# Optimization experiments

Hardware: AMD Instinct MI355X
Metric: run time of the kernel (lower is better)

## Reference

```python
import jax, jax.numpy as jnp
import numpy as np

IN_FEATURES = 1024
OUT_FEATURES = 256
NUM_KNOTS = 10
SPLINE_ORDER = 3
NUM_BASIS = NUM_KNOTS + SPLINE_ORDER  # 13
EPS = 1e-8


def setup_inputs() -> dict:
    key = jax.random.key(0)
    k1, k2 = jax.random.split(key)
    x = jax.random.normal(k1, (8192, IN_FEATURES), dtype=jnp.float32)
    spline_coeffs = jax.random.normal(
        k2, (OUT_FEATURES, IN_FEATURES, NUM_BASIS), dtype=jnp.float32) * 0.1
    knots = jnp.linspace(-1.0, 1.0, NUM_KNOTS + 2 * SPLINE_ORDER, dtype=jnp.float32)
    return {"x": x, "spline_coeffs": spline_coeffs, "knots": knots}


def _basis_functions(x, knots):
    # x: (B, I) already tanh-normalized; returns (B, I, NUM_BASIS)
    xc = jnp.clip(x, -1.0, 1.0)[..., None]          # (B, I, 1)
    left = knots[:NUM_BASIS - 1]                     # (nb-1,)
    center = knots[1:NUM_BASIS]                      # (nb-1,)
    right = knots[2:NUM_BASIS + 1]                   # (nb-1,)  (i+2 < len(knots) always)
    mask_l = (xc >= left) & (xc < center)
    mask_r = (xc >= center) & (xc < right)
    up = mask_l.astype(xc.dtype) * (xc - left) / (center - left + EPS)
    down = mask_r.astype(xc.dtype) * (right - xc) / (right - center + EPS)
    b = up + down                                    # (B, I, nb-1)
    # last basis column is never written in the original loop -> zeros
    return jnp.pad(b, ((0, 0), (0, 0), (0, 1)))


def reference(x, spline_coeffs, knots):
    x_norm = jnp.tanh(x)
    basis = _basis_functions(x_norm, knots)          # (B, I, K)
    # output[b, j] = sum_i sum_k basis[b, i, k] * coeffs[j, i, k]
    return jnp.einsum('bik,jik->bj', basis, spline_coeffs)
```

## Files before the change

kernel.cpp:

```cpp
#include <hip/hip_runtime.h>
#include <cstdint>
#include <cstddef>


typedef _Float16 half2_v __attribute__((ext_vector_type(2)));
typedef __fp16  fp16x2  __attribute__((ext_vector_type(2)));
typedef _Float16 f16x8 __attribute__((ext_vector_type(8)));
typedef float f32x4 __attribute__((ext_vector_type(4)));

__device__ __forceinline__ half2_v u32_as_h2(uint32_t u) {
  union { uint32_t u; half2_v h; } c; c.u = u; return c.h;
}
__device__ __forceinline__ uint32_t h2_as_u32(half2_v h) {
  union { uint32_t u; half2_v h; } c; c.h = h; return c.u;
}
__device__ __forceinline__ half2_v cvt_pk_h2(float a, float b) {
  union { fp16x2 f; half2_v h; } c;
  c.f = __builtin_amdgcn_cvt_pkrtz(a, b);
  return c.h;
}
__device__ __forceinline__ float dot2f(half2_v a, half2_v b, float c) {
#if __has_builtin(__builtin_amdgcn_fdot2)
  return __builtin_amdgcn_fdot2(a, b, c, false);
#else
  return c + (float)a[0] * (float)b[0] + (float)a[1] * (float)b[1];
#endif
}
__device__ __forceinline__ uint16_t f16_bits(float v) {
  union { _Float16 h; uint16_t u; } c; c.h = (_Float16)v; return c.u;
}

__device__ __forceinline__ float fast_tanhf(float v) {
  const float e = __expf(2.0f * v);
  return 1.0f - 2.0f / (e + 1.0f);
}

#define KSTEP 0.13333333333333333f
#define KINV  7.49999943750004f
__device__ __forceinline__ void kan_weights(float xin, float& w0, float& w1, int& lo) {
  float xc = fast_tanhf(xin);
  xc = fminf(fmaxf(xc, -1.0f), 1.0f);
  int m = (int)((xc + 1.0f) * 7.5f);
  m = min(max(m, 0), 14);
  const float k0 = fmaf((float)m, KSTEP, -1.0f);
  const float up = (xc - k0) * KINV;
  const float dn = (k0 + KSTEP - xc) * KINV;
  w0 = (m == 0) ? up : ((m <= 12) ? dn : 0.0f);
  w1 = (m >= 1 && m <= 11) ? up : 0.0f;
  lo = min(max(m - 1, 0), 11);
}

__device__ __forceinline__ void load_lds16(const void* g, void* l) {
  __builtin_amdgcn_global_load_lds((const __attribute__((address_space(1))) void*)g,
                                   (__attribute__((address_space(3))) void*)l, 16, 0, 0);
}

#define GMM 8192
#define GNN 256
#define KI  12
#define GK2 (1024 * KI)
#define KSPL2 2
#define IPER (1024 / KSPL2)
#define BM2 64
#define BN2 256
#define NSG 64
#define NSTEP 192
#define AS_STRIDE 208
#define AS_SG (64 * AS_STRIDE)
#define OUT_ELEMS (8192 * 256)

__global__ __launch_bounds__(256)
void kan_prep_B2(const float* __restrict__ coef, uint32_t* __restrict__ B2,
                 float4* __restrict__ outz, int zero_out) {
  const int tid = blockIdx.x * 256 + threadIdx.x;
  const float* cp = coef + (size_t)tid * 13;
  uint32_t w[6];
#pragma unroll
  for (int q = 0; q < 6; ++q) w[q] = h2_as_u32(cvt_pk_h2(cp[2 * q], cp[2 * q + 1]));
  uint2* p = (uint2*)(B2 + (size_t)tid * 6);
  p[0] = make_uint2(w[0], w[1]);
  p[1] = make_uint2(w[2], w[3]);
  p[2] = make_uint2(w[4], w[5]);
  if (zero_out) {
    const float4 z = make_float4(0.f, 0.f, 0.f, 0.f);
    outz[tid] = z;
    outz[tid + 262144] = z;
  }
}

__global__ __launch_bounds__(256)
void kan_reduce2(const float4* __restrict__ part, float4* __restrict__ out) {
  const int i = blockIdx.x * 256 + threadIdx.x;
  out[i] = make_float4(part[i].x + part[i + OUT_ELEMS / 4].x,
                       part[i].y + part[i + OUT_ELEMS / 4].y,
                       part[i].z + part[i + OUT_ELEMS / 4].z,
                       part[i].w + part[i + OUT_ELEMS / 4].w);
}

__global__ __launch_bounds__(512, 2)
void kan_gemm13(const float* __restrict__ x, const _Float16* __restrict__ B2,
                float* __restrict__ out, float* __restrict__ part, int mode) {
  __shared__ __align__(16) char Bs[4][16384];
  __shared__ __align__(16) char As[2][AS_SG];
  char* BsP = (char*)Bs;
  char* AsP = (char*)As;

  const int t    = threadIdx.x;
  const int lane = t & 63;
  const int wv   = t >> 6;
  const int wm   = (wv & 1) * 32;
  const int wn   = (wv >> 1) * 64;
  const int fr   = lane & 15;
  const int fq   = lane >> 4;
  const int m0   = blockIdx.z * BM2;
  const int i00  = blockIdx.x * IPER;

  const int a_base = (wm + fr) * AS_STRIDE + fq * 16;
  const int b_base = (wn + fr) * 64 + ((fq ^ (fr & 3)) * 16);

  f32x4 acc[2][4];
#pragma unroll
  for (int a = 0; a < 2; ++a)
#pragma unroll
    for (int b = 0; b < 4; ++b) acc[a][b] = (f32x4){0.f, 0.f, 0.f, 0.f};

  const int srow0 = t >> 2, sc0 = t & 3;
  const int srow1 = 128 + (t >> 2);
  const _Float16* sp0 = B2 + (size_t)srow0 * GK2 + (size_t)i00 * KI
                        + ((sc0 ^ (srow0 & 3)) * 8);
  const _Float16* sp1 = B2 + (size_t)srow1 * GK2 + (size_t)i00 * KI
                        + ((sc0 ^ (srow1 & 3)) * 8);

  const int xrow  = t & 63;
  const int i_loc = t >> 6;
  const float* xptr = x + (size_t)(m0 + xrow) * 1024 + i00 + i_loc;
  const int exp_off = xrow * AS_STRIDE + i_loc * 24;

  auto expand1 = [&](int dst, float xv) {
    float w0, w1; int lo;
    kan_weights(xv, w0, w1, lo);
    const uint32_t wp  = (uint32_t)f16_bits(w0) | ((uint32_t)f16_bits(w1) << 16);
    const uint32_t wlo = (lo & 1) ? (wp << 16) : wp;
    const uint32_t whi = (lo & 1) ? (wp >> 16) : 0u;
    const int w   = lo >> 1;
    const int wn1 = (w + 1 > 5) ? 5 : (w + 1);
    char* rb = AsP + dst + exp_off;
    if ((i_loc & 1) == 0) {
      *(uint4*)(rb)      = make_uint4(0u, 0u, 0u, 0u);
      *(uint2*)(rb + 16) = make_uint2(0u, 0u);
    } else {
      *(uint2*)(rb)      = make_uint2(0u, 0u);
      *(uint4*)(rb + 8)  = make_uint4(0u, 0u, 0u, 0u);
    }
    *(uint32_t*)(rb + wn1 * 4) = whi;
    *(uint32_t*)(rb + w * 4)   = wlo;
  };

  float cx, nx = 0.f;

  {
    const float ex = xptr[0];
    load_lds16(sp0, BsP + t * 16);
    load_lds16(sp1, BsP + 8192 + t * 16);
    sp0 += 32; sp1 += 32;
    load_lds16(sp0, BsP + 16384 + t * 16);
    load_lds16(sp1, BsP + 16384 + 8192 + t * 16);
    sp0 += 32; sp1 += 32;
    expand1(0, ex);
    cx = xptr[8];
  }
  asm volatile("s_waitcnt vmcnt(2) lgkmcnt(0)" ::: "memory");
  __builtin_amdgcn_s_barrier();
  __builtin_amdgcn_sched_barrier(0);

#define GRANP(U, PH, XPF)                                                     \
  {                                                                           \
    const int g = 12 * B + 3 * (U) + (PH);                                    \
    const char* Asrc = AsP + ((U) & 1) * AS_SG;                               \
    f16x8 af0 = *(const f16x8*)(Asrc + a_base + (PH) * 64);                   \
    f16x8 af1 = *(const f16x8*)(Asrc + a_base + (PH) * 64 + 16 * AS_STRIDE);  \
    load_lds16(sp0, BsP + ((3 * (U) + (PH) + 2) & 3) * 16384 + t * 16);       \
    load_lds16(sp1, BsP + ((3 * (U) + (PH) + 2) & 3) * 16384 + 8192 + t * 16);\
    { const int adv = (g + 3 <= NSTEP - 1) ? 32 : 0; sp0 += adv; sp1 += adv; }\
    XPF                                                                       \
    if ((PH) == 0 && (4 * B + (U)) < NSG - 1)                                 \
      expand1((((U) + 1) & 1) * AS_SG, cx);                                   \
    asm volatile("s_waitcnt vmcnt(3) lgkmcnt(0)" ::: "memory");               \
    __builtin_amdgcn_s_barrier();                                             \
    __builtin_amdgcn_sched_barrier(0);                                        \
    __builtin_amdgcn_s_setprio(1);                                            \
    _Pragma("unroll")                                                         \
    for (int ni = 0; ni < 4; ++ni) {                                          \
      const f16x8 bf = *(const f16x8*)(BsP + ((3 * (U) + (PH)) & 3) * 16384   \
                                       + b_base + ni * 1024);                 \
      acc[0][ni] = __builtin_amdgcn_mfma_f32_16x16x32_f16(af0, bf, acc[0][ni], 0, 0, 0); \
      acc[1][ni] = __builtin_amdgcn_mfma_f32_16x16x32_f16(af1, bf, acc[1][ni], 0, 0, 0); \
    }                                                                         \
    __builtin_amdgcn_s_setprio(0);                                            \
  }

#define SGBODY(U)                                                             \
  {                                                                           \
    const int sgp = 4 * B + (U) + 2;                                          \
    const int sgn = (sgp < NSG) ? sgp : (NSG - 1);                            \
    GRANP(U, 0, { })                                                          \
    GRANP(U, 1, { nx = xptr[8 * sgn]; })                                      \
    GRANP(U, 2, { })                                                          \
    cx = nx;                                                                  \
  }

  for (int B = 0; B < 16; ++B) {
    SGBODY(0)
    SGBODY(1)
    SGBODY(2)
    SGBODY(3)
  }
#undef SGBODY
#undef GRANP

  if (mode) {
    float* pb = part + (size_t)blockIdx.x * OUT_ELEMS;
#pragma unroll
    for (int q = 0; q < 2; ++q) {
      const int gr = m0 + wm + q * 16 + fq * 4;
#pragma unroll
      for (int ni = 0; ni < 4; ++ni) {
        const int gc = wn + ni * 16 + fr;
#pragma unroll
        for (int r = 0; r < 4; ++r)
          pb[(size_t)(gr + r) * GNN + gc] = acc[q][ni][r];
      }
    }
  } else {
#pragma unroll
    for (int q = 0; q < 2; ++q) {
      const int gr = m0 + wm + q * 16 + fq * 4;
#pragma unroll
      for (int ni = 0; ni < 4; ++ni) {
        const int gc = wn + ni * 16 + fr;
#pragma unroll
        for (int r = 0; r < 4; ++r)
          atomicAdd(&out[(size_t)(gr + r) * GNN + gc], acc[q][ni][r]);
      }
    }
  }
}

#define TI 8
#define BT 256
#define JT 32
#define ISPL 2
#define IRANGE (1024 / ISPL)

__global__ __launch_bounds__(256)
void kan_dot2(const float* __restrict__ x, const float* __restrict__ coef,
              float* __restrict__ out) {
  __shared__ uint32_t Plds[TI * 12 * JT];
  const int t    = threadIdx.x;
  const int b    = blockIdx.x * BT + t;
  const int j0   = blockIdx.y * JT;
  const int cbeg = blockIdx.z * (IRANGE / TI);

  float acc[JT];
#pragma unroll
  for (int q = 0; q < JT; ++q) acc[q] = 0.0f;

  const int s_jj   = t & 31;
  const int s_iloc = t >> 5;

  for (int c = cbeg; c < cbeg + IRANGE / TI; ++c) {
    const int i0 = c * TI;
    __syncthreads();
    {
      const float* cp0 = coef + ((size_t)(j0 + s_jj) * 1024 + (i0 + s_iloc)) * 13;
      float cv[13];
#pragma unroll
      for (int s = 0; s < 13; ++s) cv[s] = cp0[s];
#pragma unroll
      for (int r = 0; r < 12; ++r) {
        half2_v h; h[0] = (_Float16)cv[r]; h[1] = (_Float16)cv[r + 1];
        const int slot = ((s_jj >> 2) + r) & 7;
        Plds[(s_iloc * 12 + r) * 32 + slot * 4 + (s_jj & 3)] = h2_as_u32(h);
      }
    }
    uint32_t wr[TI]; int lor[TI];
    {
      const float* xr = x + (size_t)b * 1024 + i0;
      const float4 xa = *(const float4*)(xr);
      const float4 xb = *(const float4*)(xr + 4);
      const float xv[TI] = {xa.x, xa.y, xa.z, xa.w, xb.x, xb.y, xb.z, xb.w};
#pragma unroll
      for (int q = 0; q < TI; ++q) {
        float w0, w1; int lo;
        kan_weights(xv[q], w0, w1, lo);
        wr[q] = (uint32_t)f16_bits(w0) | ((uint32_t)f16_bits(w1) << 16);
        lor[q] = lo;
      }
    }
    __syncthreads();

    const uint4* P4 = (const uint4*)Plds;
#pragma unroll
    for (int ii = 0; ii < TI; ++ii) {
      const half2_v hw = u32_as_h2(wr[ii]);
      const int lo = lor[ii];
      const int base = (ii * 12 + lo) * 8;
#pragma unroll
      for (int g = 0; g < 8; ++g) {
        const uint4 v = P4[base + ((g + lo) & 7)];
        acc[4 * g + 0] = dot2f(hw, u32_as_h2(v.x), acc[4 * g + 0]);
        acc[4 * g + 1] = dot2f(hw, u32_as_h2(v.y), acc[4 * g + 1]);
        acc[4 * g + 2] = dot2f(hw, u32_as_h2(v.z), acc[4 * g + 2]);
        acc[4 * g + 3] = dot2f(hw, u32_as_h2(v.w), acc[4 * g + 3]);
      }
    }
  }

  float* orow = out + (size_t)b * 256 + j0;
#pragma unroll
  for (int q = 0; q < JT; ++q) atomicAdd(orow + q, acc[q]);
}

extern "C" void kernel_launch(void* const* d_in, const int* in_sizes, int n_in,
                              void* d_out, int out_size, void* d_ws, size_t ws_size,
                              hipStream_t stream) {
  const float* x     = (const float*)d_in[0];
  const float* coef  = (const float*)d_in[1];
  float* out = (float*)d_out;

  const size_t b2_bytes   = (size_t)GNN * GK2 * 2;
  const size_t part_off   = b2_bytes;
  const size_t part_bytes = (size_t)KSPL2 * OUT_ELEMS * 4;

  if (ws_size >= part_off + part_bytes) {
    _Float16* B2 = (_Float16*)d_ws;
    float* part  = (float*)((char*)d_ws + part_off);
    kan_prep_B2<<<1024, 256, 0, stream>>>(coef, (uint32_t*)B2, (float4*)out, 0);
    dim3 grid(KSPL2, 1, GMM / BM2);
    kan_gemm13<<<grid, 512, 0, stream>>>(x, B2, out, part, 1);
    kan_reduce2<<<OUT_ELEMS / 4 / 256, 256, 0, stream>>>((const float4*)part,
                                                         (float4*)out);
  } else if (ws_size >= b2_bytes) {
    _Float16* B2 = (_Float16*)d_ws;
    kan_prep_B2<<<1024, 256, 0, stream>>>(coef, (uint32_t*)B2, (float4*)out, 1);
    dim3 grid(KSPL2, 1, GMM / BM2);
    kan_gemm13<<<grid, 512, 0, stream>>>(x, B2, out, nullptr, 0);
  } else {
    (void)hipMemsetAsync(out, 0, (size_t)out_size * sizeof(float), stream);
    dim3 grid(8192 / BT, 256 / JT, ISPL);
    kan_dot2<<<grid, 256, 0, stream>>>(x, coef, out);
  }
}
```

Measured before the change: 187.5 us.

## Split N across blocks: 256-thread 64x128 tiles with four waves each

Each GEMM block now covers a 64x128 output tile with 256 threads instead of 64x256 with 512 threads, and the grid gains an N-split dimension. Each wave computes all 64 rows by 32 columns, so it issues four A fragment loads and reuses each B fragment across four MFMAs. The basis expansion of x is spread over two phases because there are fewer threads. The aims are more blocks per CU, smaller LDS per block, better occupancy and latency hiding, and the x prefetch now runs after the barrier. The cost is that every x row is expanded twice (once per N half) and A is reread more often from LDS.

```diff
diff --git a/kernel.cpp b/kernel.cpp
--- a/kernel.cpp
+++ b/kernel.cpp
@@ -60,12 +60,14 @@
 #define KI  12
 #define GK2 (1024 * KI)
 #define KSPL2 2
+#define NSPL2 2
 #define IPER (1024 / KSPL2)
 #define BM2 64
-#define BN2 256
+#define BN2 128
 #define NSG 64
 #define NSTEP 192
-#define AS_STRIDE 208
+#define BS_TILE 8192
+#define AS_STRIDE 200
 #define AS_SG (64 * AS_STRIDE)
 #define OUT_ELEMS (8192 * 256)
 
@@ -97,10 +99,10 @@
                        part[i].w + part[i + OUT_ELEMS / 4].w);
 }
 
-__global__ __launch_bounds__(512, 2)
-void kan_gemm13(const float* __restrict__ x, const _Float16* __restrict__ B2,
+__global__ __launch_bounds__(256, 4)
+void kan_gemm14(const float* __restrict__ x, const _Float16* __restrict__ B2,
                 float* __restrict__ out, float* __restrict__ part, int mode) {
-  __shared__ __align__(16) char Bs[4][16384];
+  __shared__ __align__(16) char Bs[4][BS_TILE];
   __shared__ __align__(16) char As[2][AS_SG];
   char* BsP = (char*)Bs;
   char* AsP = (char*)As;
@@ -108,35 +110,34 @@
   const int t    = threadIdx.x;
   const int lane = t & 63;
   const int wv   = t >> 6;
-  const int wm   = (wv & 1) * 32;
-  const int wn   = (wv >> 1) * 64;
+  const int wn   = wv * 32;
   const int fr   = lane & 15;
   const int fq   = lane >> 4;
   const int m0   = blockIdx.z * BM2;
+  const int n0   = blockIdx.y * BN2;
   const int i00  = blockIdx.x * IPER;
 
-  const int a_base = (wm + fr) * AS_STRIDE + fq * 16;
+  const int a_base = fr * AS_STRIDE + fq * 16;
   const int b_base = (wn + fr) * 64 + ((fq ^ (fr & 3)) * 16);
 
-  f32x4 acc[2][4];
-#pragma unroll
-  for (int a = 0; a < 2; ++a)
-#pragma unroll
-    for (int b = 0; b < 4; ++b) acc[a][b] = (f32x4){0.f, 0.f, 0.f, 0.f};
+  f32x4 acc[4][2];
+#pragma unroll
+  for (int a = 0; a < 4; ++a)
+#pragma unroll
+    for (int b = 0; b < 2; ++b) acc[a][b] = (f32x4){0.f, 0.f, 0.f, 0.f};
 
   const int srow0 = t >> 2, sc0 = t & 3;
-  const int srow1 = 128 + (t >> 2);
-  const _Float16* sp0 = B2 + (size_t)srow0 * GK2 + (size_t)i00 * KI
+  const int srow1 = 64 + (t >> 2);
+  const _Float16* sp0 = B2 + (size_t)(n0 + srow0) * GK2 + (size_t)i00 * KI
                         + ((sc0 ^ (srow0 & 3)) * 8);
-  const _Float16* sp1 = B2 + (size_t)srow1 * GK2 + (size_t)i00 * KI
+  const _Float16* sp1 = B2 + (size_t)(n0 + srow1) * GK2 + (size_t)i00 * KI
                         + ((sc0 ^ (srow1 & 3)) * 8);
 
   const int xrow  = t & 63;
   const int i_loc = t >> 6;
   const float* xptr = x + (size_t)(m0 + xrow) * 1024 + i00 + i_loc;
-  const int exp_off = xrow * AS_STRIDE + i_loc * 24;
-
-  auto expand1 = [&](int dst, float xv) {
+
+  auto expand1 = [&](int dst, float xv, int il) {
     float w0, w1; int lo;
     kan_weights(xv, w0, w1, lo);
     const uint32_t wp  = (uint32_t)f16_bits(w0) | ((uint32_t)f16_bits(w1) << 16);
@@ -144,8 +145,8 @@
     const uint32_t whi = (lo & 1) ? (wp >> 16) : 0u;
     const int w   = lo >> 1;
     const int wn1 = (w + 1 > 5) ? 5 : (w + 1);
-    char* rb = AsP + dst + exp_off;
-    if ((i_loc & 1) == 0) {
+    char* rb = AsP + dst + xrow * AS_STRIDE + il * 24;
+    if ((il & 1) == 0) {
       *(uint4*)(rb)      = make_uint4(0u, 0u, 0u, 0u);
       *(uint2*)(rb + 16) = make_uint2(0u, 0u);
     } else {
@@ -156,20 +157,23 @@
     *(uint32_t*)(rb + w * 4)   = wlo;
   };
 
-  float cx, nx = 0.f;
+  float cxa, cxb, nxa = 0.f, nxb = 0.f;
 
   {
-    const float ex = xptr[0];
+    const float exa = xptr[0];
+    const float exb = xptr[4];
     load_lds16(sp0, BsP + t * 16);
-    load_lds16(sp1, BsP + 8192 + t * 16);
+    load_lds16(sp1, BsP + (256 + t) * 16);
     sp0 += 32; sp1 += 32;
-    load_lds16(sp0, BsP + 16384 + t * 16);
-    load_lds16(sp1, BsP + 16384 + 8192 + t * 16);
+    load_lds16(sp0, BsP + BS_TILE + t * 16);
+    load_lds16(sp1, BsP + BS_TILE + (256 + t) * 16);
     sp0 += 32; sp1 += 32;
-    expand1(0, ex);
-    cx = xptr[8];
-  }
-  asm volatile("s_waitcnt vmcnt(2) lgkmcnt(0)" ::: "memory");
+    expand1(0, exa, i_loc);
+    expand1(0, exb, i_loc + 4);
+    cxa = xptr[8];
+    cxb = xptr[12];
+  }
+  asm volatile("s_waitcnt vmcnt(0) lgkmcnt(0)" ::: "memory");
   __builtin_amdgcn_s_barrier();
   __builtin_amdgcn_sched_barrier(0);
 
@@ -179,22 +183,28 @@
     const char* Asrc = AsP + ((U) & 1) * AS_SG;                               \
     f16x8 af0 = *(const f16x8*)(Asrc + a_base + (PH) * 64);                   \
     f16x8 af1 = *(const f16x8*)(Asrc + a_base + (PH) * 64 + 16 * AS_STRIDE);  \
-    load_lds16(sp0, BsP + ((3 * (U) + (PH) + 2) & 3) * 16384 + t * 16);       \
-    load_lds16(sp1, BsP + ((3 * (U) + (PH) + 2) & 3) * 16384 + 8192 + t * 16);\
+    f16x8 af2 = *(const f16x8*)(Asrc + a_base + (PH) * 64 + 32 * AS_STRIDE);  \
+    f16x8 af3 = *(const f16x8*)(Asrc + a_base + (PH) * 64 + 48 * AS_STRIDE);  \
+    load_lds16(sp0, BsP + ((3 * (U) + (PH) + 2) & 3) * BS_TILE + t * 16);     \
+    load_lds16(sp1, BsP + ((3 * (U) + (PH) + 2) & 3) * BS_TILE + (256 + t) * 16); \
     { const int adv = (g + 3 <= NSTEP - 1) ? 32 : 0; sp0 += adv; sp1 += adv; }\
-    XPF                                                                       \
     if ((PH) == 0 && (4 * B + (U)) < NSG - 1)                                 \
-      expand1((((U) + 1) & 1) * AS_SG, cx);                                   \
-    asm volatile("s_waitcnt vmcnt(3) lgkmcnt(0)" ::: "memory");               \
+      expand1((((U) + 1) & 1) * AS_SG, cxa, i_loc);                           \
+    if ((PH) == 1 && (4 * B + (U)) < NSG - 1)                                 \
+      expand1((((U) + 1) & 1) * AS_SG, cxb, i_loc + 4);                       \
+    asm volatile("s_waitcnt vmcnt(4) lgkmcnt(0)" ::: "memory");               \
     __builtin_amdgcn_s_barrier();                                             \
     __builtin_amdgcn_sched_barrier(0);                                        \
+    XPF                                                                       \
     __builtin_amdgcn_s_setprio(1);                                            \
     _Pragma("unroll")                                                         \
-    for (int ni = 0; ni < 4; ++ni) {                                          \
-      const f16x8 bf = *(const f16x8*)(BsP + ((3 * (U) + (PH)) & 3) * 16384   \
+    for (int ni = 0; ni < 2; ++ni) {                                          \
+      const f16x8 bf = *(const f16x8*)(BsP + ((3 * (U) + (PH)) & 3) * BS_TILE \
                                        + b_base + ni * 1024);                 \
       acc[0][ni] = __builtin_amdgcn_mfma_f32_16x16x32_f16(af0, bf, acc[0][ni], 0, 0, 0); \
       acc[1][ni] = __builtin_amdgcn_mfma_f32_16x16x32_f16(af1, bf, acc[1][ni], 0, 0, 0); \
+      acc[2][ni] = __builtin_amdgcn_mfma_f32_16x16x32_f16(af2, bf, acc[2][ni], 0, 0, 0); \
+      acc[3][ni] = __builtin_amdgcn_mfma_f32_16x16x32_f16(af3, bf, acc[3][ni], 0, 0, 0); \
     }                                                                         \
     __builtin_amdgcn_s_setprio(0);                                            \
   }
@@ -204,9 +214,9 @@
     const int sgp = 4 * B + (U) + 2;                                          \
     const int sgn = (sgp < NSG) ? sgp : (NSG - 1);                            \
     GRANP(U, 0, { })                                                          \
-    GRANP(U, 1, { nx = xptr[8 * sgn]; })                                      \
+    GRANP(U, 1, { nxa = xptr[8 * sgn]; nxb = xptr[8 * sgn + 4]; })            \
     GRANP(U, 2, { })                                                          \
-    cx = nx;                                                                  \
+    cxa = nxa; cxb = nxb;                                                     \
   }
 
   for (int B = 0; B < 16; ++B) {
@@ -221,11 +231,11 @@
   if (mode) {
     float* pb = part + (size_t)blockIdx.x * OUT_ELEMS;
 #pragma unroll
-    for (int q = 0; q < 2; ++q) {
-      const int gr = m0 + wm + q * 16 + fq * 4;
-#pragma unroll
-      for (int ni = 0; ni < 4; ++ni) {
-        const int gc = wn + ni * 16 + fr;
+    for (int q = 0; q < 4; ++q) {
+      const int gr = m0 + q * 16 + fq * 4;
+#pragma unroll
+      for (int ni = 0; ni < 2; ++ni) {
+        const int gc = n0 + wn + ni * 16 + fr;
 #pragma unroll
         for (int r = 0; r < 4; ++r)
           pb[(size_t)(gr + r) * GNN + gc] = acc[q][ni][r];
@@ -233,11 +243,11 @@
     }
   } else {
 #pragma unroll
-    for (int q = 0; q < 2; ++q) {
-      const int gr = m0 + wm + q * 16 + fq * 4;
-#pragma unroll
-      for (int ni = 0; ni < 4; ++ni) {
-        const int gc = wn + ni * 16 + fr;
+    for (int q = 0; q < 4; ++q) {
+      const int gr = m0 + q * 16 + fq * 4;
+#pragma unroll
+      for (int ni = 0; ni < 2; ++ni) {
+        const int gc = n0 + wn + ni * 16 + fr;
 #pragma unroll
         for (int r = 0; r < 4; ++r)
           atomicAdd(&out[(size_t)(gr + r) * GNN + gc], acc[q][ni][r]);
@@ -336,15 +346,15 @@
     _Float16* B2 = (_Float16*)d_ws;
     float* part  = (float*)((char*)d_ws + part_off);
     kan_prep_B2<<<1024, 256, 0, stream>>>(coef, (uint32_t*)B2, (float4*)out, 0);
-    dim3 grid(KSPL2, 1, GMM / BM2);
-    kan_gemm13<<<grid, 512, 0, stream>>>(x, B2, out, part, 1);
+    dim3 grid(KSPL2, NSPL2, GMM / BM2);
+    kan_gemm14<<<grid, 256, 0, stream>>>(x, B2, out, part, 1);
     kan_reduce2<<<OUT_ELEMS / 4 / 256, 256, 0, stream>>>((const float4*)part,
                                                          (float4*)out);
   } else if (ws_size >= b2_bytes) {
     _Float16* B2 = (_Float16*)d_ws;
     kan_prep_B2<<<1024, 256, 0, stream>>>(coef, (uint32_t*)B2, (float4*)out, 1);
-    dim3 grid(KSPL2, 1, GMM / BM2);
-    kan_gemm13<<<grid, 512, 0, stream>>>(x, B2, out, nullptr, 0);
+    dim3 grid(KSPL2, NSPL2, GMM / BM2);
+    kan_gemm14<<<grid, 256, 0, stream>>>(x, B2, out, nullptr, 0);
   } else {
     (void)hipMemsetAsync(out, 0, (size_t)out_size * sizeof(float), stream);
     dim3 grid(8192 / BT, 256 / JT, ISPL);
```

Result: slower. 315.2 us (+68.1%).

## Fuse split-K reduction into GEMM via ticket counter; coalesce coeff prep through LDS

Applied to the files above, without the earlier changes.

Removes the separate reduce kernel launch: each GEMM block writes its partial tile, then a per-row-tile atomic ticket lets whichever of the two split-K blocks finishes second sum both partials into the output. The prep kernel now stages the 13-float coefficient records through shared memory with coalesced float4 loads instead of strided scalar reads, and resets the ticket counters. The ticket scheme adds threadfences and a serialized tail on the last block, and it relies on memory ordering across blocks for correctness.

```diff
diff --git a/kernel.cpp b/kernel.cpp
--- a/kernel.cpp
+++ b/kernel.cpp
@@ -69,39 +69,43 @@
 #define AS_SG (64 * AS_STRIDE)
 #define OUT_ELEMS (8192 * 256)
 
-__global__ __launch_bounds__(256)
+__global__ __launch_bounds__(512)
 void kan_prep_B2(const float* __restrict__ coef, uint32_t* __restrict__ B2,
-                 float4* __restrict__ outz, int zero_out) {
-  const int tid = blockIdx.x * 256 + threadIdx.x;
-  const float* cp = coef + (size_t)tid * 13;
+                 float4* __restrict__ outz, unsigned* __restrict__ ticket,
+                 int zero_out) {
+  __shared__ float Cl[512 * 13];
+  const int t    = threadIdx.x;
+  const int rec0 = blockIdx.x * 512;
+  const float4* src = (const float4*)(coef + (size_t)rec0 * 13);
+  float4* dl = (float4*)Cl;
+  dl[t]        = src[t];
+  dl[t + 512]  = src[t + 512];
+  dl[t + 1024] = src[t + 1024];
+  if (t < 128) dl[t + 1536] = src[t + 1536];
+  __syncthreads();
+  const float* cp = Cl + t * 13;
   uint32_t w[6];
 #pragma unroll
   for (int q = 0; q < 6; ++q) w[q] = h2_as_u32(cvt_pk_h2(cp[2 * q], cp[2 * q + 1]));
-  uint2* p = (uint2*)(B2 + (size_t)tid * 6);
+  uint2* p = (uint2*)(B2 + (size_t)(rec0 + t) * 6);
   p[0] = make_uint2(w[0], w[1]);
   p[1] = make_uint2(w[2], w[3]);
   p[2] = make_uint2(w[4], w[5]);
   if (zero_out) {
     const float4 z = make_float4(0.f, 0.f, 0.f, 0.f);
-    outz[tid] = z;
-    outz[tid + 262144] = z;
-  }
-}
-
-__global__ __launch_bounds__(256)
-void kan_reduce2(const float4* __restrict__ part, float4* __restrict__ out) {
-  const int i = blockIdx.x * 256 + threadIdx.x;
-  out[i] = make_float4(part[i].x + part[i + OUT_ELEMS / 4].x,
-                       part[i].y + part[i + OUT_ELEMS / 4].y,
-                       part[i].z + part[i + OUT_ELEMS / 4].z,
-                       part[i].w + part[i + OUT_ELEMS / 4].w);
+    outz[blockIdx.x * 1024 + t] = z;
+    outz[blockIdx.x * 1024 + 512 + t] = z;
+  }
+  if (ticket != nullptr && blockIdx.x == 0 && t < 128) ticket[t] = 0u;
 }
 
 __global__ __launch_bounds__(512, 2)
-void kan_gemm13(const float* __restrict__ x, const _Float16* __restrict__ B2,
-                float* __restrict__ out, float* __restrict__ part, int mode) {
+void kan_gemm16(const float* __restrict__ x, const _Float16* __restrict__ B2,
+                float* __restrict__ out, float* __restrict__ part,
+                unsigned* __restrict__ ticket, int mode) {
   __shared__ __align__(16) char Bs[4][16384];
   __shared__ __align__(16) char As[2][AS_SG];
+  __shared__ unsigned s_flag;
   char* BsP = (char*)Bs;
   char* AsP = (char*)As;
 
@@ -231,6 +235,23 @@
           pb[(size_t)(gr + r) * GNN + gc] = acc[q][ni][r];
       }
     }
+    __threadfence();
+    __syncthreads();
+    if (t == 0) s_flag = atomicAdd(&ticket[blockIdx.z], 1u);
+    __syncthreads();
+    if (s_flag == 1u) {
+      __threadfence();
+      const float4* p0 = (const float4*)part + (size_t)m0 * 64;
+      const float4* p1 = (const float4*)(part + OUT_ELEMS) + (size_t)m0 * 64;
+      float4* ob = (float4*)out + (size_t)m0 * 64;
+#pragma unroll
+      for (int q = 0; q < 8; ++q) {
+        const int idx = q * 512 + t;
+        const float4 a = p0[idx];
+        const float4 b = p1[idx];
+        ob[idx] = make_float4(a.x + b.x, a.y + b.y, a.z + b.z, a.w + b.w);
+      }
+    }
   } else {
 #pragma unroll
     for (int q = 0; q < 2; ++q) {
@@ -331,20 +352,22 @@
   const size_t b2_bytes   = (size_t)GNN * GK2 * 2;
   const size_t part_off   = b2_bytes;
   const size_t part_bytes = (size_t)KSPL2 * OUT_ELEMS * 4;
-
-  if (ws_size >= part_off + part_bytes) {
+  const size_t tick_off   = part_off + part_bytes;
+  const size_t tick_bytes = 128 * sizeof(unsigned);
+
+  if (ws_size >= tick_off + tick_bytes) {
     _Float16* B2 = (_Float16*)d_ws;
     float* part  = (float*)((char*)d_ws + part_off);
-    kan_prep_B2<<<1024, 256, 0, stream>>>(coef, (uint32_t*)B2, (float4*)out, 0);
+    unsigned* tk = (unsigned*)((char*)d_ws + tick_off);
+    kan_prep_B2<<<512, 512, 0, stream>>>(coef, (uint32_t*)B2, (float4*)out, tk, 0);
     dim3 grid(KSPL2, 1, GMM / BM2);
-    kan_gemm13<<<grid, 512, 0, stream>>>(x, B2, out, part, 1);
-    kan_reduce2<<<OUT_ELEMS / 4 / 256, 256, 0, stream>>>((const float4*)part,
-                                                         (float4*)out);
+    kan_gemm16<<<grid, 512, 0, stream>>>(x, B2, out, part, tk, 1);
   } else if (ws_size >= b2_bytes) {
     _Float16* B2 = (_Float16*)d_ws;
-    kan_prep_B2<<<1024, 256, 0, stream>>>(coef, (uint32_t*)B2, (float4*)out, 1);
+    kan_prep_B2<<<512, 512, 0, stream>>>(coef, (uint32_t*)B2, (float4*)out,
+                                         nullptr, 1);
     dim3 grid(KSPL2, 1, GMM / BM2);
-    kan_gemm13<<<grid, 512, 0, stream>>>(x, B2, out, nullptr, 0);
+    kan_gemm16<<<grid, 512, 0, stream>>>(x, B2, out, nullptr, nullptr, 0);
   } else {
     (void)hipMemsetAsync(out, 0, (size_t)out_size * sizeof(float), stream);
     dim3 grid(8192 / BT, 256 / JT, ISPL);
```

Measured after the change: 281.1 us. +49.9%, slower.
